# Optimization experiments

Measured on AMD Instinct MI355X. Metric: run time of the kernel, lower is better.

Reference implementation:

```python
import jax, jax.numpy as jnp
import numpy as np

N, K, D = 8192, 4096, 256


def setup_inputs() -> dict:
    key = jax.random.key(0)
    kx, kc, kw = jax.random.split(key, 3)
    x = jax.random.normal(kx, (N, D), dtype=jnp.float32)
    centers = jax.random.normal(kc, (K, D), dtype=jnp.float32)
    w = jax.random.normal(kw, (K,), dtype=jnp.float32)
    # bandwidth chosen so exp(-sigma * d2) stays in a healthy range for
    # Gaussian data where E[||x-c||^2] ~= 2*D
    sigma = jnp.asarray(1.0 / (2.0 * D), dtype=jnp.float32)
    return {"x": x, "centers": centers, "w": w, "sigma": sigma}


def reference(x, centers, w, sigma):
    # phi[n,k] = exp(-sigma * ||x_n - c_k||^2), computed via the GEMM
    x2 = jnp.sum(x * x, axis=-1, keepdims=True)          # [N,1]
    c2 = jnp.sum(centers * centers, axis=-1)             # [K]
    d2 = x2 + c2 - 2.0 * jnp.einsum('nd,kd->nk', x, centers)  # [N,K]
    d2 = jnp.maximum(d2, 0.0)  # clamp tiny negative round-off
    phi = jnp.exp(-sigma * d2)                           # [N,K]
    # (w * phi).sum(1) == phi @ w
    return jnp.einsum('nk,k->n', phi, w)                 # [N]
```

## Files before the change

### kernel.cpp

```cpp
#include <hip/hip_runtime.h>

#define NROWS 8192
#define NCENT 4096
#define DIM   256

#define AS1 __attribute__((address_space(1)))
#define AS3 __attribute__((address_space(3)))

typedef short bf16x8 __attribute__((ext_vector_type(8)));
typedef float f32x4  __attribute__((ext_vector_type(4)));

__device__ inline unsigned short f2bf(float f) {
    unsigned u = __float_as_uint(f);
    return (unsigned short)((u + 0x7fffu + ((u >> 16) & 1u)) >> 16);
}

__global__ __launch_bounds__(256) void prep_kernel(const float* __restrict__ x,
                                                   const float* __restrict__ c,
                                                   float* __restrict__ norms,
                                                   unsigned short* __restrict__ xbf,
                                                   unsigned short* __restrict__ cbf) {
    const int t = threadIdx.x, lane = t & 63;
    const int wbase = (blockIdx.x * 4 + (t >> 6)) * 4;
    #pragma unroll
    for (int rr = 0; rr < 4; ++rr) {
        const int gw = wbase + rr;
        const float* src;
        unsigned short* dst;
        if (gw < NROWS) { src = x + (size_t)gw * DIM;           dst = xbf + (size_t)gw * DIM; }
        else            { src = c + (size_t)(gw - NROWS) * DIM; dst = cbf + (size_t)(gw - NROWS) * DIM; }
        float4 v = ((const float4*)src)[lane];
        ushort4 b;
        b.x = f2bf(v.x); b.y = f2bf(v.y); b.z = f2bf(v.z); b.w = f2bf(v.w);
        ((ushort4*)dst)[lane] = b;
        float s = v.x * v.x + v.y * v.y + v.z * v.z + v.w * v.w;
        #pragma unroll
        for (int m = 32; m; m >>= 1) s += __shfl_xor(s, m);
        if (lane == 0) norms[gw] = s;
    }
}

#define BUFS (256 * 32)

__global__ __launch_bounds__(512, 2) void rbf_mfma256(const unsigned short* __restrict__ xbf,
                                                      const unsigned short* __restrict__ cbf,
                                                      const float* __restrict__ w,
                                                      const float* __restrict__ sigp,
                                                      const float* __restrict__ norms,
                                                      float* __restrict__ out) {
    __shared__ __align__(16) short As[2 * BUFS];
    __shared__ __align__(16) short Bs[2 * BUFS];

    const int t    = threadIdx.x;
    const int wave = t >> 6, lane = t & 63;

    const int bid = blockIdx.x;
    const int swz = (bid & 7) * 64 + (bid >> 3);
    const int m0  = (swz >> 4) * 256;
    const int n0  = (swz & 15) * 256;

    const int wy = wave >> 2, wx = wave & 3;
    const int lr = lane & 15;
    const int g  = lane >> 4;

    const int r_in = lane >> 2;
    const int c_l  = (lane & 3) ^ ((r_in >> 1) & 3);
    const unsigned short* ga0 = xbf + (size_t)(m0 + 32 * wave + r_in) * DIM + c_l * 8;
    const unsigned short* ga1 = ga0 + 16 * DIM;
    const unsigned short* gb0 = cbf + (size_t)(n0 + 32 * wave + r_in) * DIM + c_l * 8;
    const unsigned short* gb1 = gb0 + 16 * DIM;
    short* la0 = As + (32 * wave) * 32;
    short* lb0 = Bs + (32 * wave) * 32;

#define STAGE(buf, kk) do {                                                                             \
        const int ko_ = (kk) * 32;                                                                      \
        __builtin_amdgcn_global_load_lds((const AS1 void*)(ga0 + ko_),                                  \
                                         (AS3 void*)(la0 + (buf) * BUFS), 16, 0, 0);                    \
        __builtin_amdgcn_global_load_lds((const AS1 void*)(ga1 + ko_),                                  \
                                         (AS3 void*)(la0 + (buf) * BUFS + 16 * 32), 16, 0, 0);          \
        __builtin_amdgcn_global_load_lds((const AS1 void*)(gb0 + ko_),                                  \
                                         (AS3 void*)(lb0 + (buf) * BUFS), 16, 0, 0);                    \
        __builtin_amdgcn_global_load_lds((const AS1 void*)(gb1 + ko_),                                  \
                                         (AS3 void*)(lb0 + (buf) * BUFS + 16 * 32), 16, 0, 0);          \
    } while (0)

    int aoff[8], boff[4];
    #pragma unroll
    for (int i = 0; i < 8; ++i) {
        int r = 128 * wy + 16 * i + lr;
        aoff[i] = r * 32 + ((g ^ ((r >> 1) & 3)) * 8);
    }
    #pragma unroll
    for (int j = 0; j < 4; ++j) {
        int r = 64 * wx + 16 * j + lr;
        boff[j] = r * 32 + ((g ^ ((r >> 1) & 3)) * 8);
    }

    f32x4 acc[8][4];
    #pragma unroll
    for (int i = 0; i < 8; ++i)
        #pragma unroll
        for (int j = 0; j < 4; ++j) acc[i][j] = f32x4{0, 0, 0, 0};

    STAGE(0, 0);

    #pragma unroll
    for (int kk = 0; kk < 8; ++kk) {
        const int cur = kk & 1;
        if (kk < 7) {
            STAGE(cur ^ 1, kk + 1);
            asm volatile("s_waitcnt vmcnt(4)" ::: "memory");
        } else {
            asm volatile("s_waitcnt vmcnt(0)" ::: "memory");
        }
        __builtin_amdgcn_s_barrier();
        __builtin_amdgcn_sched_barrier(0);

        const short* Ab = As + cur * BUFS;
        const short* Bb = Bs + cur * BUFS;
        bf16x8 a[8], b[4];
        #pragma unroll
        for (int i = 0; i < 8; ++i) a[i] = *(const bf16x8*)(Ab + aoff[i]);
        #pragma unroll
        for (int j = 0; j < 4; ++j) b[j] = *(const bf16x8*)(Bb + boff[j]);
        #pragma unroll
        for (int i = 0; i < 8; ++i)
            #pragma unroll
            for (int j = 0; j < 4; ++j)
                acc[i][j] = __builtin_amdgcn_mfma_f32_16x16x32_bf16(a[i], b[j], acc[i][j], 0, 0, 0);

        __builtin_amdgcn_sched_barrier(0);
        __builtin_amdgcn_s_barrier();
    }
#undef STAGE

    const float sigma = sigp[0];
    const float* x2 = norms;
    const float* c2 = norms + NROWS;

    float c2v[4], wv[4];
    #pragma unroll
    for (int j = 0; j < 4; ++j) {
        int n = n0 + 64 * wx + 16 * j + lr;
        c2v[j] = c2[n];
        wv[j]  = w[n];
    }

    #pragma unroll
    for (int i = 0; i < 8; ++i) {
        const int mbase = m0 + 128 * wy + 16 * i + 4 * g;
        float4 x2v = *(const float4*)(x2 + mbase);
        float rs[4] = {0.f, 0.f, 0.f, 0.f};
        #pragma unroll
        for (int j = 0; j < 4; ++j) {
            #pragma unroll
            for (int r = 0; r < 4; ++r) {
                float x2r = (r == 0) ? x2v.x : (r == 1) ? x2v.y : (r == 2) ? x2v.z : x2v.w;
                float d2 = x2r + c2v[j] - 2.0f * acc[i][j][r];
                d2 = fmaxf(d2, 0.0f);
                rs[r] += wv[j] * __expf(-sigma * d2);
            }
        }
        #pragma unroll
        for (int r = 0; r < 4; ++r) {
            rs[r] += __shfl_xor(rs[r], 1);
            rs[r] += __shfl_xor(rs[r], 2);
            rs[r] += __shfl_xor(rs[r], 4);
            rs[r] += __shfl_xor(rs[r], 8);
        }
        if (lr == 0) {
            #pragma unroll
            for (int r = 0; r < 4; ++r) atomicAdd(&out[mbase + r], rs[r]);
        }
    }
}

__global__ __launch_bounds__(256) void norms_kernel(const float* __restrict__ x,
                                                    const float* __restrict__ c,
                                                    float* __restrict__ ws) {
    int t = threadIdx.x, lane = t & 63;
    int gw = blockIdx.x * 4 + (t >> 6);
    const float* src;
    float* dst;
    if (gw < NROWS) { src = x + (size_t)gw * DIM;           dst = ws + gw; }
    else            { src = c + (size_t)(gw - NROWS) * DIM; dst = ws + gw; }
    float4 v = ((const float4*)src)[lane];
    float s = v.x * v.x + v.y * v.y + v.z * v.z + v.w * v.w;
    #pragma unroll
    for (int m = 32; m; m >>= 1) s += __shfl_xor(s, m);
    if (lane == 0) *dst = s;
}

__global__ __launch_bounds__(256) void rbf_kernel(const float* __restrict__ x,
                                                  const float* __restrict__ cent,
                                                  const float* __restrict__ w,
                                                  const float* __restrict__ sigp,
                                                  const float* __restrict__ norms,
                                                  float* __restrict__ out) {
    __shared__ __align__(16) short xs[64 * 32];
    __shared__ __align__(16) short cs[64 * 32];
    const int t = threadIdx.x;
    const int m0 = blockIdx.y * 64, n0 = blockIdx.x * 64;
    const int srow = t >> 2, seg = t & 3;
    const int pchunk = seg ^ ((srow >> 1) & 3);
    const int sidx = srow * 32 + pchunk * 8;
    const float* xg = x    + (size_t)(m0 + srow) * DIM + seg * 8;
    const float* cg = cent + (size_t)(n0 + srow) * DIM + seg * 8;
    const int lane = t & 63, wave = t >> 6;
    const int lr = lane & 15, lg = lane >> 4;
    const int arow = 16 * wave + lr;
    const int aidx = arow * 32 + ((lg ^ ((arow >> 1) & 3)) * 8);
    f32x4 acc[4] = {f32x4{0,0,0,0}, f32x4{0,0,0,0}, f32x4{0,0,0,0}, f32x4{0,0,0,0}};
    for (int k0 = 0; k0 < DIM; k0 += 32) {
        float4 f0 = *(const float4*)(xg + k0);
        float4 f1 = *(const float4*)(xg + k0 + 4);
        float4 g0 = *(const float4*)(cg + k0);
        float4 g1 = *(const float4*)(cg + k0 + 4);
        __syncthreads();
        union { unsigned short s[8]; int4 v; } ux, uc;
        ux.s[0]=f2bf(f0.x); ux.s[1]=f2bf(f0.y); ux.s[2]=f2bf(f0.z); ux.s[3]=f2bf(f0.w);
        ux.s[4]=f2bf(f1.x); ux.s[5]=f2bf(f1.y); ux.s[6]=f2bf(f1.z); ux.s[7]=f2bf(f1.w);
        uc.s[0]=f2bf(g0.x); uc.s[1]=f2bf(g0.y); uc.s[2]=f2bf(g0.z); uc.s[3]=f2bf(g0.w);
        uc.s[4]=f2bf(g1.x); uc.s[5]=f2bf(g1.y); uc.s[6]=f2bf(g1.z); uc.s[7]=f2bf(g1.w);
        *(int4*)(xs + sidx) = ux.v;
        *(int4*)(cs + sidx) = uc.v;
        __syncthreads();
        bf16x8 a = *(const bf16x8*)(xs + aidx);
        #pragma unroll
        for (int bt = 0; bt < 4; ++bt) {
            const int brow = 16 * bt + lr;
            bf16x8 b = *(const bf16x8*)(cs + brow * 32 + ((lg ^ ((brow >> 1) & 3)) * 8));
            acc[bt] = __builtin_amdgcn_mfma_f32_16x16x32_bf16(a, b, acc[bt], 0, 0, 0);
        }
    }
    const float sigma = sigp[0];
    const float* x2 = norms;
    const float* c2 = norms + NROWS;
    const int rbase = m0 + 16 * wave + lg * 4;
    float x2v[4];
    #pragma unroll
    for (int r = 0; r < 4; ++r) x2v[r] = x2[rbase + r];
    float rs[4] = {0.f, 0.f, 0.f, 0.f};
    #pragma unroll
    for (int bt = 0; bt < 4; ++bt) {
        const int col = n0 + 16 * bt + lr;
        const float c2v = c2[col];
        const float wvv = w[col];
        #pragma unroll
        for (int r = 0; r < 4; ++r) {
            float d2 = x2v[r] + c2v - 2.0f * acc[bt][r];
            d2 = fmaxf(d2, 0.0f);
            rs[r] += wvv * __expf(-sigma * d2);
        }
    }
    #pragma unroll
    for (int r = 0; r < 4; ++r) {
        rs[r] += __shfl_xor(rs[r], 1);
        rs[r] += __shfl_xor(rs[r], 2);
        rs[r] += __shfl_xor(rs[r], 4);
        rs[r] += __shfl_xor(rs[r], 8);
    }
    if (lr == 0) {
        #pragma unroll
        for (int r = 0; r < 4; ++r) atomicAdd(&out[rbase + r], rs[r]);
    }
}

extern "C" void kernel_launch(void* const* d_in, const int* in_sizes, int n_in,
                              void* d_out, int out_size, void* d_ws, size_t ws_size,
                              hipStream_t stream) {
    const float* x    = (const float*)d_in[0];
    const float* cent = (const float*)d_in[1];
    const float* w    = (const float*)d_in[2];
    const float* sig  = (const float*)d_in[3];
    float* out = (float*)d_out;

    const size_t norms_elems = NROWS + NCENT;
    const size_t xbf_off  = norms_elems * sizeof(float);
    const size_t cbf_off  = xbf_off + (size_t)NROWS * DIM * sizeof(unsigned short);
    const size_t ws_need  = cbf_off + (size_t)NCENT * DIM * sizeof(unsigned short);

    hipMemsetAsync(d_out, 0, (size_t)out_size * sizeof(float), stream);

    if (ws_size >= ws_need) {
        float* norms = (float*)d_ws;
        unsigned short* xbf = (unsigned short*)((char*)d_ws + xbf_off);
        unsigned short* cbf = (unsigned short*)((char*)d_ws + cbf_off);
        prep_kernel<<<(NROWS + NCENT) / 16, 256, 0, stream>>>(x, cent, norms, xbf, cbf);
        rbf_mfma256<<<512, 512, 0, stream>>>(xbf, cbf, w, sig, norms, out);
    } else {
        float* norms = (float*)d_ws;
        norms_kernel<<<(NROWS + NCENT) / 4, 256, 0, stream>>>(x, cent, norms);
        rbf_kernel<<<dim3(NCENT / 64, NROWS / 64), 256, 0, stream>>>(x, cent, w, sig, norms, out);
    }
}
```

Measured before the change: 115.0 us.

## Deepen K-tile to 64, cut barriers, and replace atomics with partial-sum reduction

Doubles the K depth of each LDS stage from 32 to 64 with an 8-way XOR swizzle, halving the main-loop iterations and their barriers. The MFMA blocks are split into halves with s_setprio raised around them. The per-row atomicAdd epilogue and output memset are replaced by float4 stores into a 64-slice partial buffer, summed by a new reduce kernel. LDS use per block grows to about 128KB, which likely allows only one block per CU despite launch_bounds(512,2). The extra workspace need could also send execution to the slower fallback path if the workspace is too small.

```diff
diff --git a/kernel.cpp b/kernel.cpp
--- a/kernel.cpp
+++ b/kernel.cpp
@@ -40,16 +40,16 @@
     }
 }
 
-#define BUFS (256 * 32)
+#define ATILE (256 * 64)
 
 __global__ __launch_bounds__(512, 2) void rbf_mfma256(const unsigned short* __restrict__ xbf,
                                                       const unsigned short* __restrict__ cbf,
                                                       const float* __restrict__ w,
                                                       const float* __restrict__ sigp,
                                                       const float* __restrict__ norms,
-                                                      float* __restrict__ out) {
-    __shared__ __align__(16) short As[2 * BUFS];
-    __shared__ __align__(16) short Bs[2 * BUFS];
+                                                      float* __restrict__ part) {
+    __shared__ __align__(16) short As[2 * ATILE];
+    __shared__ __align__(16) short Bs[2 * ATILE];
 
     const int t    = threadIdx.x;
     const int wave = t >> 6, lane = t & 63;
@@ -63,37 +63,34 @@
     const int lr = lane & 15;
     const int g  = lane >> 4;
 
-    const int r_in = lane >> 2;
-    const int c_l  = (lane & 3) ^ ((r_in >> 1) & 3);
-    const unsigned short* ga0 = xbf + (size_t)(m0 + 32 * wave + r_in) * DIM + c_l * 8;
-    const unsigned short* ga1 = ga0 + 16 * DIM;
-    const unsigned short* gb0 = cbf + (size_t)(n0 + 32 * wave + r_in) * DIM + c_l * 8;
-    const unsigned short* gb1 = gb0 + 16 * DIM;
-    short* la0 = As + (32 * wave) * 32;
-    short* lb0 = Bs + (32 * wave) * 32;
-
-#define STAGE(buf, kk) do {                                                                             \
-        const int ko_ = (kk) * 32;                                                                      \
-        __builtin_amdgcn_global_load_lds((const AS1 void*)(ga0 + ko_),                                  \
-                                         (AS3 void*)(la0 + (buf) * BUFS), 16, 0, 0);                    \
-        __builtin_amdgcn_global_load_lds((const AS1 void*)(ga1 + ko_),                                  \
-                                         (AS3 void*)(la0 + (buf) * BUFS + 16 * 32), 16, 0, 0);          \
-        __builtin_amdgcn_global_load_lds((const AS1 void*)(gb0 + ko_),                                  \
-                                         (AS3 void*)(lb0 + (buf) * BUFS), 16, 0, 0);                    \
-        __builtin_amdgcn_global_load_lds((const AS1 void*)(gb1 + ko_),                                  \
-                                         (AS3 void*)(lb0 + (buf) * BUFS + 16 * 32), 16, 0, 0);          \
+    const int rsub = lane >> 3;
+    const int csw  = (lane & 7) ^ rsub;
+    const unsigned short* gaw = xbf + (size_t)(m0 + 32 * wave + rsub) * DIM + csw * 8;
+    const unsigned short* gbw = cbf + (size_t)(n0 + 32 * wave + rsub) * DIM + csw * 8;
+
+#define STAGE(buf, tt) do {                                                                              \
+        const int ko_ = (tt) * 64;                                                                       \
+        _Pragma("unroll")                                                                                \
+        for (int l_ = 0; l_ < 4; ++l_) {                                                                 \
+            __builtin_amdgcn_global_load_lds((const AS1 void*)(gaw + ko_ + l_ * 8 * DIM),                \
+                                             (AS3 void*)(As + (buf) * ATILE + (32 * wave + 8 * l_) * 64),\
+                                             16, 0, 0);                                                  \
+            __builtin_amdgcn_global_load_lds((const AS1 void*)(gbw + ko_ + l_ * 8 * DIM),                \
+                                             (AS3 void*)(Bs + (buf) * ATILE + (32 * wave + 8 * l_) * 64),\
+                                             16, 0, 0);                                                  \
+        }                                                                                                \
     } while (0)
 
     int aoff[8], boff[4];
     #pragma unroll
     for (int i = 0; i < 8; ++i) {
         int r = 128 * wy + 16 * i + lr;
-        aoff[i] = r * 32 + ((g ^ ((r >> 1) & 3)) * 8);
+        aoff[i] = r * 64 + ((g ^ (r & 7)) * 8);
     }
     #pragma unroll
     for (int j = 0; j < 4; ++j) {
         int r = 64 * wx + 16 * j + lr;
-        boff[j] = r * 32 + ((g ^ ((r >> 1) & 3)) * 8);
+        boff[j] = r * 64 + ((g ^ (r & 7)) * 8);
     }
 
     f32x4 acc[8][4];
@@ -103,40 +100,62 @@
         for (int j = 0; j < 4; ++j) acc[i][j] = f32x4{0, 0, 0, 0};
 
     STAGE(0, 0);
-
-    #pragma unroll
-    for (int kk = 0; kk < 8; ++kk) {
-        const int cur = kk & 1;
-        if (kk < 7) {
-            STAGE(cur ^ 1, kk + 1);
-            asm volatile("s_waitcnt vmcnt(4)" ::: "memory");
-        } else {
+    asm volatile("s_waitcnt vmcnt(0)" ::: "memory");
+    __builtin_amdgcn_s_barrier();
+    __builtin_amdgcn_sched_barrier(0);
+
+    #pragma unroll
+    for (int kt = 0; kt < 4; ++kt) {
+        const int buf = kt & 1;
+        if (kt < 3) STAGE(buf ^ 1, kt + 1);
+        __builtin_amdgcn_sched_barrier(0);
+
+        const short* Ab = As + buf * ATILE;
+        const short* Bb = Bs + buf * ATILE;
+
+        #pragma unroll
+        for (int h = 0; h < 2; ++h) {
+            bf16x8 a[4][2];
+            #pragma unroll
+            for (int i = 0; i < 4; ++i) {
+                a[i][0] = *(const bf16x8*)(Ab + aoff[4 * h + i]);
+                a[i][1] = *(const bf16x8*)(Ab + (aoff[4 * h + i] ^ 32));
+            }
+            #pragma unroll
+            for (int q = 0; q < 2; ++q) {
+                const int jb = 2 * (h ? 1 - q : q);
+                bf16x8 b[2][2];
+                #pragma unroll
+                for (int jj = 0; jj < 2; ++jj) {
+                    b[jj][0] = *(const bf16x8*)(Bb + boff[jb + jj]);
+                    b[jj][1] = *(const bf16x8*)(Bb + (boff[jb + jj] ^ 32));
+                }
+                __builtin_amdgcn_s_setprio(1);
+                #pragma unroll
+                for (int i = 0; i < 4; ++i)
+                    #pragma unroll
+                    for (int jj = 0; jj < 2; ++jj) {
+                        acc[4 * h + i][jb + jj] =
+                            __builtin_amdgcn_mfma_f32_16x16x32_bf16(a[i][0], b[jj][0], acc[4 * h + i][jb + jj], 0, 0, 0);
+                        acc[4 * h + i][jb + jj] =
+                            __builtin_amdgcn_mfma_f32_16x16x32_bf16(a[i][1], b[jj][1], acc[4 * h + i][jb + jj], 0, 0, 0);
+                    }
+                __builtin_amdgcn_s_setprio(0);
+            }
+        }
+
+        if (kt < 3) {
             asm volatile("s_waitcnt vmcnt(0)" ::: "memory");
-        }
-        __builtin_amdgcn_s_barrier();
-        __builtin_amdgcn_sched_barrier(0);
-
-        const short* Ab = As + cur * BUFS;
-        const short* Bb = Bs + cur * BUFS;
-        bf16x8 a[8], b[4];
-        #pragma unroll
-        for (int i = 0; i < 8; ++i) a[i] = *(const bf16x8*)(Ab + aoff[i]);
-        #pragma unroll
-        for (int j = 0; j < 4; ++j) b[j] = *(const bf16x8*)(Bb + boff[j]);
-        #pragma unroll
-        for (int i = 0; i < 8; ++i)
-            #pragma unroll
-            for (int j = 0; j < 4; ++j)
-                acc[i][j] = __builtin_amdgcn_mfma_f32_16x16x32_bf16(a[i], b[j], acc[i][j], 0, 0, 0);
-
-        __builtin_amdgcn_sched_barrier(0);
-        __builtin_amdgcn_s_barrier();
+            __builtin_amdgcn_s_barrier();
+            __builtin_amdgcn_sched_barrier(0);
+        }
     }
 #undef STAGE
 
     const float sigma = sigp[0];
     const float* x2 = norms;
     const float* c2 = norms + NROWS;
+    const int sl = (n0 >> 8) * 4 + wx;
 
     float c2v[4], wv[4];
     #pragma unroll
@@ -169,10 +188,19 @@
             rs[r] += __shfl_xor(rs[r], 8);
         }
         if (lr == 0) {
-            #pragma unroll
-            for (int r = 0; r < 4; ++r) atomicAdd(&out[mbase + r], rs[r]);
-        }
-    }
+            float4 v = make_float4(rs[0], rs[1], rs[2], rs[3]);
+            *(float4*)(part + (size_t)sl * NROWS + mbase) = v;
+        }
+    }
+}
+
+__global__ __launch_bounds__(256) void reduce_kernel(const float* __restrict__ part,
+                                                     float* __restrict__ out) {
+    const int m = blockIdx.x * 256 + threadIdx.x;
+    float s = 0.f;
+    #pragma unroll
+    for (int p = 0; p < 64; ++p) s += part[(size_t)p * NROWS + m];
+    out[m] = s;
 }
 
 __global__ __launch_bounds__(256) void norms_kernel(const float* __restrict__ x,
@@ -278,18 +306,20 @@
     const size_t norms_elems = NROWS + NCENT;
     const size_t xbf_off  = norms_elems * sizeof(float);
     const size_t cbf_off  = xbf_off + (size_t)NROWS * DIM * sizeof(unsigned short);
-    const size_t ws_need  = cbf_off + (size_t)NCENT * DIM * sizeof(unsigned short);
-
-    hipMemsetAsync(d_out, 0, (size_t)out_size * sizeof(float), stream);
+    const size_t part_off = cbf_off + (size_t)NCENT * DIM * sizeof(unsigned short);
+    const size_t ws_need  = part_off + (size_t)64 * NROWS * sizeof(float);
 
     if (ws_size >= ws_need) {
         float* norms = (float*)d_ws;
         unsigned short* xbf = (unsigned short*)((char*)d_ws + xbf_off);
         unsigned short* cbf = (unsigned short*)((char*)d_ws + cbf_off);
+        float* part = (float*)((char*)d_ws + part_off);
         prep_kernel<<<(NROWS + NCENT) / 16, 256, 0, stream>>>(x, cent, norms, xbf, cbf);
-        rbf_mfma256<<<512, 512, 0, stream>>>(xbf, cbf, w, sig, norms, out);
+        rbf_mfma256<<<512, 512, 0, stream>>>(xbf, cbf, w, sig, norms, part);
+        reduce_kernel<<<NROWS / 256, 256, 0, stream>>>(part, out);
     } else {
         float* norms = (float*)d_ws;
+        hipMemsetAsync(d_out, 0, (size_t)out_size * sizeof(float), stream);
         norms_kernel<<<(NROWS + NCENT) / 4, 256, 0, stream>>>(x, cent, norms);
         rbf_kernel<<<dim3(NCENT / 64, NROWS / 64), 256, 0, stream>>>(x, cent, w, sig, norms, out);
     }
```

Result: no change. 114.8 us (-0.2%).

## Deepen LDS pipeline to four stages and replace atomics with partial-sum reduction

Applied to the files above, without the earlier changes.

Moves the GEMM main loop from double buffering to a four-slot LDS ring that keeps three K-tiles in flight. The trailing barrier is dropped, and MFMA issue priority is raised with s_setprio. The epilogue now writes per-column-slice partial row sums to a workspace buffer and a new reduce kernel sums them. This removes the output memset and the global atomics. The cost is double the LDS per block, which likely no longer fits two blocks per CU, plus a larger workspace requirement and an extra kernel launch.

```diff
diff --git a/kernel.cpp b/kernel.cpp
--- a/kernel.cpp
+++ b/kernel.cpp
@@ -40,16 +40,16 @@
     }
 }
 
-#define BUFS (256 * 32)
+#define SLOT (256 * 32)
 
 __global__ __launch_bounds__(512, 2) void rbf_mfma256(const unsigned short* __restrict__ xbf,
                                                       const unsigned short* __restrict__ cbf,
                                                       const float* __restrict__ w,
                                                       const float* __restrict__ sigp,
                                                       const float* __restrict__ norms,
-                                                      float* __restrict__ out) {
-    __shared__ __align__(16) short As[2 * BUFS];
-    __shared__ __align__(16) short Bs[2 * BUFS];
+                                                      float* __restrict__ part) {
+    __shared__ __align__(16) short As[4 * SLOT];
+    __shared__ __align__(16) short Bs[4 * SLOT];
 
     const int t    = threadIdx.x;
     const int wave = t >> 6, lane = t & 63;
@@ -72,16 +72,16 @@
     short* la0 = As + (32 * wave) * 32;
     short* lb0 = Bs + (32 * wave) * 32;
 
-#define STAGE(buf, kk) do {                                                                             \
-        const int ko_ = (kk) * 32;                                                                      \
-        __builtin_amdgcn_global_load_lds((const AS1 void*)(ga0 + ko_),                                  \
-                                         (AS3 void*)(la0 + (buf) * BUFS), 16, 0, 0);                    \
-        __builtin_amdgcn_global_load_lds((const AS1 void*)(ga1 + ko_),                                  \
-                                         (AS3 void*)(la0 + (buf) * BUFS + 16 * 32), 16, 0, 0);          \
-        __builtin_amdgcn_global_load_lds((const AS1 void*)(gb0 + ko_),                                  \
-                                         (AS3 void*)(lb0 + (buf) * BUFS), 16, 0, 0);                    \
-        __builtin_amdgcn_global_load_lds((const AS1 void*)(gb1 + ko_),                                  \
-                                         (AS3 void*)(lb0 + (buf) * BUFS + 16 * 32), 16, 0, 0);          \
+#define STAGE(s, kk) do {                                                                   \
+        const int ko_ = (kk) * 32;                                                          \
+        __builtin_amdgcn_global_load_lds((const AS1 void*)(ga0 + ko_),                      \
+                                         (AS3 void*)(la0 + (s) * SLOT), 16, 0, 0);          \
+        __builtin_amdgcn_global_load_lds((const AS1 void*)(ga1 + ko_),                      \
+                                         (AS3 void*)(la0 + (s) * SLOT + 16 * 32), 16, 0, 0);\
+        __builtin_amdgcn_global_load_lds((const AS1 void*)(gb0 + ko_),                      \
+                                         (AS3 void*)(lb0 + (s) * SLOT), 16, 0, 0);          \
+        __builtin_amdgcn_global_load_lds((const AS1 void*)(gb1 + ko_),                      \
+                                         (AS3 void*)(lb0 + (s) * SLOT + 16 * 32), 16, 0, 0);\
     } while (0)
 
     int aoff[8], boff[4];
@@ -103,40 +103,42 @@
         for (int j = 0; j < 4; ++j) acc[i][j] = f32x4{0, 0, 0, 0};
 
     STAGE(0, 0);
-
-    #pragma unroll
-    for (int kk = 0; kk < 8; ++kk) {
-        const int cur = kk & 1;
-        if (kk < 7) {
-            STAGE(cur ^ 1, kk + 1);
-            asm volatile("s_waitcnt vmcnt(4)" ::: "memory");
-        } else {
-            asm volatile("s_waitcnt vmcnt(0)" ::: "memory");
-        }
+    STAGE(1, 1);
+    STAGE(2, 2);
+    __builtin_amdgcn_sched_barrier(0);
+
+    #pragma unroll
+    for (int kt = 0; kt < 8; ++kt) {
+        if (kt <= 5)      asm volatile("s_waitcnt vmcnt(8)" ::: "memory");
+        else if (kt == 6) asm volatile("s_waitcnt vmcnt(4)" ::: "memory");
+        else              asm volatile("s_waitcnt vmcnt(0)" ::: "memory");
         __builtin_amdgcn_s_barrier();
         __builtin_amdgcn_sched_barrier(0);
 
-        const short* Ab = As + cur * BUFS;
-        const short* Bb = Bs + cur * BUFS;
+        if (kt <= 4) STAGE((kt + 3) & 3, kt + 3);
+        __builtin_amdgcn_sched_barrier(0);
+
+        const short* Ab = As + (kt & 3) * SLOT;
+        const short* Bb = Bs + (kt & 3) * SLOT;
         bf16x8 a[8], b[4];
         #pragma unroll
         for (int i = 0; i < 8; ++i) a[i] = *(const bf16x8*)(Ab + aoff[i]);
         #pragma unroll
         for (int j = 0; j < 4; ++j) b[j] = *(const bf16x8*)(Bb + boff[j]);
+        __builtin_amdgcn_s_setprio(1);
         #pragma unroll
         for (int i = 0; i < 8; ++i)
             #pragma unroll
             for (int j = 0; j < 4; ++j)
                 acc[i][j] = __builtin_amdgcn_mfma_f32_16x16x32_bf16(a[i], b[j], acc[i][j], 0, 0, 0);
-
-        __builtin_amdgcn_sched_barrier(0);
-        __builtin_amdgcn_s_barrier();
+        __builtin_amdgcn_s_setprio(0);
     }
 #undef STAGE
 
     const float sigma = sigp[0];
     const float* x2 = norms;
     const float* c2 = norms + NROWS;
+    const int sl = (n0 >> 8) * 4 + wx;
 
     float c2v[4], wv[4];
     #pragma unroll
@@ -169,10 +171,19 @@
             rs[r] += __shfl_xor(rs[r], 8);
         }
         if (lr == 0) {
-            #pragma unroll
-            for (int r = 0; r < 4; ++r) atomicAdd(&out[mbase + r], rs[r]);
-        }
-    }
+            float4 v = make_float4(rs[0], rs[1], rs[2], rs[3]);
+            *(float4*)(part + (size_t)sl * NROWS + mbase) = v;
+        }
+    }
+}
+
+__global__ __launch_bounds__(256) void reduce_kernel(const float* __restrict__ part,
+                                                     float* __restrict__ out) {
+    const int m = blockIdx.x * 256 + threadIdx.x;
+    float s = 0.f;
+    #pragma unroll
+    for (int p = 0; p < 64; ++p) s += part[(size_t)p * NROWS + m];
+    out[m] = s;
 }
 
 __global__ __launch_bounds__(256) void norms_kernel(const float* __restrict__ x,
@@ -278,18 +289,20 @@
     const size_t norms_elems = NROWS + NCENT;
     const size_t xbf_off  = norms_elems * sizeof(float);
     const size_t cbf_off  = xbf_off + (size_t)NROWS * DIM * sizeof(unsigned short);
-    const size_t ws_need  = cbf_off + (size_t)NCENT * DIM * sizeof(unsigned short);
-
-    hipMemsetAsync(d_out, 0, (size_t)out_size * sizeof(float), stream);
+    const size_t part_off = cbf_off + (size_t)NCENT * DIM * sizeof(unsigned short);
+    const size_t ws_need  = part_off + (size_t)64 * NROWS * sizeof(float);
 
     if (ws_size >= ws_need) {
         float* norms = (float*)d_ws;
         unsigned short* xbf = (unsigned short*)((char*)d_ws + xbf_off);
         unsigned short* cbf = (unsigned short*)((char*)d_ws + cbf_off);
+        float* part = (float*)((char*)d_ws + part_off);
         prep_kernel<<<(NROWS + NCENT) / 16, 256, 0, stream>>>(x, cent, norms, xbf, cbf);
-        rbf_mfma256<<<512, 512, 0, stream>>>(xbf, cbf, w, sig, norms, out);
+        rbf_mfma256<<<512, 512, 0, stream>>>(xbf, cbf, w, sig, norms, part);
+        reduce_kernel<<<NROWS / 256, 256, 0, stream>>>(part, out);
     } else {
         float* norms = (float*)d_ws;
+        hipMemsetAsync(d_out, 0, (size_t)out_size * sizeof(float), stream);
         norms_kernel<<<(NROWS + NCENT) / 4, 256, 0, stream>>>(x, cent, norms);
         rbf_kernel<<<dim3(NCENT / 64, NROWS / 64), 256, 0, stream>>>(x, cent, w, sig, norms, out);
     }
```

New measurement: 116.6 us. Within noise of the previous version (+1.4%).
